# Optimization experiments

Measured on AMD Instinct MI355X. Metric: run time of the kernel, lower is better.

Reference implementation:

```python
import jax, jax.numpy as jnp
import numpy as np

N, E, D, H, C = 50000, 1600000, 256, 8, 32

def setup_inputs() -> dict:
    key = jax.random.key(0)
    ks = jax.random.split(key, 7)
    feat = jax.random.normal(ks[0], (N, D), dtype=jnp.float32)
    edge_weight = jax.random.uniform(ks[1], (E,), dtype=jnp.float32)
    W_lin = jax.random.normal(ks[2], (D, H * C), dtype=jnp.float32) * (1.0 / np.sqrt(D))
    att_l = jax.random.normal(ks[3], (1, H, C), dtype=jnp.float32) * (1.0 / np.sqrt(H))
    att_r = jax.random.normal(ks[4], (1, H, C), dtype=jnp.float32) * (1.0 / np.sqrt(H))
    W_res = jax.random.normal(ks[5], (D, H * C), dtype=jnp.float32) * (1.0 / np.sqrt(D))
    edge_index = jax.random.randint(ks[6], (2, E), 0, N, dtype=jnp.int32)
    return {"feat": feat, "edge_weight": edge_weight, "W_lin": W_lin,
            "att_l": att_l, "att_r": att_r, "W_res": W_res, "edge_index": edge_index}

def reference(feat, edge_weight, W_lin, att_l, att_r, W_res, edge_index):
    n_nodes = feat.shape[0]
    h, c = att_l.shape[1], att_l.shape[2]
    src, dst = edge_index[0], edge_index[1]
    # node projection: [N, H, C]
    x = (feat @ W_lin).reshape(n_nodes, h, c)
    alpha_l = (x * att_l).sum(-1)  # [N, H]
    alpha_r = (x * att_r).sum(-1)  # [N, H]
    # per-edge scores [E, H]
    alpha = alpha_l[src] + alpha_r[dst]
    alpha = edge_weight[:, None] * alpha
    alpha = jnp.where(alpha > 0, alpha, 0.2 * alpha)  # leaky_relu(0.2)
    # segment softmax over destination nodes
    amax = jax.lax.stop_gradient(jax.ops.segment_max(alpha, dst, num_segments=n_nodes))
    ex = jnp.exp(alpha - amax[dst])
    denom = jax.ops.segment_sum(ex, dst, num_segments=n_nodes)
    coeff = ex / (denom[dst] + 1e-16)  # [E, H]
    # weighted message aggregation
    msg = x[src] * coeff[:, :, None]  # [E, H, C]
    agg = jax.ops.segment_sum(msg, dst, num_segments=n_nodes)  # [N, H, C]
    out = jax.nn.elu(agg).reshape(n_nodes, h * c)
    out = out + feat @ W_res  # residual
    return out
```

## Files before the change

kernel.cpp:

```cpp
#include <hip/hip_runtime.h>
#include <stdint.h>

#define D_DIM 256
#define NPAD  640

typedef __bf16 bf16x8 __attribute__((ext_vector_type(8)));
typedef float  f32x4  __attribute__((ext_vector_type(4)));

__device__ __forceinline__ float bf2f(unsigned short u) {
  union { unsigned int i; float f; } cv; cv.i = ((unsigned int)u) << 16; return cv.f;
}
__device__ __forceinline__ unsigned short f2bf(float f) {
  union { float f; unsigned int i; } cv; cv.f = f;
  unsigned int i = cv.i;
  unsigned int lsb = (i >> 16) & 1u;
  i += 0x7fffu + lsb;
  return (unsigned short)(i >> 16);
}
__device__ __forceinline__ void gld16(const void* gptr, void* lptr) {
  __builtin_amdgcn_global_load_lds(
      (const __attribute__((address_space(1))) unsigned int*)gptr,
      (__attribute__((address_space(3))) unsigned int*)lptr, 16, 0, 0);
}

__global__ __launch_bounds__(256) void setup_cvt_prep(
    const float* __restrict__ feat, unsigned short* __restrict__ fb,
    const float* __restrict__ W_lin, const float* __restrict__ W_res,
    const float* __restrict__ att_l, const float* __restrict__ att_r,
    unsigned short* __restrict__ Bt, int nelem, int nb_cvt) {
  int bid = blockIdx.x, t = threadIdx.x;
  if (bid < nb_cvt) {
    int i = (bid * 256 + t) * 8;
    if (i >= nelem) return;
    float4 v0 = *(const float4*)(feat + i);
    float4 v1 = *(const float4*)(feat + i + 4);
    ushort4 a, b;
    a.x = f2bf(v0.x); a.y = f2bf(v0.y); a.z = f2bf(v0.z); a.w = f2bf(v0.w);
    b.x = f2bf(v1.x); b.y = f2bf(v1.y); b.z = f2bf(v1.z); b.w = f2bf(v1.w);
    *(ushort4*)(fb + i) = a;
    *(ushort4*)(fb + i + 4) = b;
  } else {
    int idx = (bid - nb_cvt) * 256 + t;
    int n = idx >> 8, k = idx & 255;
    float v = 0.f;
    if (n < 256) v = W_lin[k * 256 + n];
    else if (n < 512) v = W_res[k * 256 + (n - 256)];
    else if (n < 520) {
      int h = n - 512; float s = 0.f;
      #pragma unroll
      for (int c = 0; c < 32; ++c) s += W_lin[k * 256 + h * 32 + c] * att_l[h * 32 + c];
      v = s;
    } else if (n < 528) {
      int h = n - 520; float s = 0.f;
      #pragma unroll
      for (int c = 0; c < 32; ++c) s += W_lin[k * 256 + h * 32 + c] * att_r[h * 32 + c];
      v = s;
    }
    Bt[idx] = f2bf(v);
  }
}

__global__ __launch_bounds__(256) void scan_partial(const int* __restrict__ cnt,
                                                    int* __restrict__ bsum, int N) {
  __shared__ int s[256];
  int t = threadIdx.x;
  int i = blockIdx.x * 256 + t;
  s[t] = (i < N) ? cnt[i] : 0;
  __syncthreads();
  for (int off = 128; off > 0; off >>= 1) {
    if (t < off) s[t] += s[t + off];
    __syncthreads();
  }
  if (t == 0) bsum[blockIdx.x] = s[0];
}

__global__ __launch_bounds__(256) void scan_top(int* __restrict__ bsum, int nb) {
  __shared__ int s[256];
  int t = threadIdx.x;
  int v = (t < nb) ? bsum[t] : 0;
  s[t] = v;
  __syncthreads();
  for (int off = 1; off < 256; off <<= 1) {
    int u = (t >= off) ? s[t - off] : 0;
    __syncthreads();
    s[t] += u;
    __syncthreads();
  }
  if (t < nb) bsum[t] = s[t] - v;
}

__global__ __launch_bounds__(256) void scan_apply(const int* __restrict__ cnt,
                                                  const int* __restrict__ bsum,
                                                  int* __restrict__ row_ptr, int N) {
  __shared__ int s[256];
  int t = threadIdx.x;
  int i = blockIdx.x * 256 + t;
  int v = (i < N) ? cnt[i] : 0;
  s[t] = v;
  __syncthreads();
  for (int off = 1; off < 256; off <<= 1) {
    int u = (t >= off) ? s[t - off] : 0;
    __syncthreads();
    s[t] += u;
    __syncthreads();
  }
  int excl = bsum[blockIdx.x] + s[t] - v;
  if (i < N) {
    row_ptr[i] = excl;
    if (i == N - 1) row_ptr[N] = excl + v;
  }
}

__global__ __launch_bounds__(256) void gemm_hist(
    const unsigned short* __restrict__ A,
    const unsigned short* __restrict__ Bt,
    float* __restrict__ out, unsigned short* __restrict__ xbf,
    float* __restrict__ alpha_l, float* __restrict__ alpha_r, int M,
    const int* __restrict__ dst, int* __restrict__ cnt, int* __restrict__ rank,
    int E, int nb_hist, int gx) {
  __shared__ unsigned short As[128 * 32];
  __shared__ unsigned short Bs[128 * 32];

  if ((int)blockIdx.x < nb_hist) {
    int base = (int)blockIdx.x * 2048 + threadIdx.x;
    #pragma unroll
    for (int u = 0; u < 8; ++u) {
      int e = base + u * 256;
      if (e < E) rank[e] = atomicAdd(&cnt[dst[e]], 1);
    }
    return;
  }

  int tid  = threadIdx.x;
  int w    = tid >> 6, lane = tid & 63;
  int gb   = (int)blockIdx.x - nb_hist;
  int bm   = (gb % gx) * 128, bn = (gb / gx) * 128;
  int wm   = (w & 1) * 64, wn = (w >> 1) * 64;
  int l16  = lane & 15, quad = lane >> 4;

  f32x4 acc[4][4] = {};

  int srow = w * 32 + (lane >> 2);
  int koff = (lane & 3) * 8;

  for (int k0 = 0; k0 < 256; k0 += 32) {
    #pragma unroll
    for (int i = 0; i < 2; ++i) {
      int r  = srow + i * 16;
      int rg = bm + r; if (rg > M - 1) rg = M - 1;
      gld16(A  + (size_t)rg * 256 + k0 + koff, &As[(w * 32 + i * 16) * 32]);
      gld16(Bt + (size_t)(bn + r) * 256 + k0 + koff, &Bs[(w * 32 + i * 16) * 32]);
    }
    __syncthreads();
    bf16x8 a[4], b[4];
    #pragma unroll
    for (int mi = 0; mi < 4; ++mi)
      a[mi] = *(const bf16x8*)&As[(wm + mi * 16 + l16) * 32 + quad * 8];
    #pragma unroll
    for (int ni = 0; ni < 4; ++ni)
      b[ni] = *(const bf16x8*)&Bs[(wn + ni * 16 + l16) * 32 + quad * 8];
    #pragma unroll
    for (int mi = 0; mi < 4; ++mi)
      #pragma unroll
      for (int ni = 0; ni < 4; ++ni)
        acc[mi][ni] = __builtin_amdgcn_mfma_f32_16x16x32_bf16(a[mi], b[ni], acc[mi][ni], 0, 0, 0);
    __syncthreads();
  }

  #pragma unroll
  for (int mi = 0; mi < 4; ++mi) {
    #pragma unroll
    for (int r = 0; r < 4; ++r) {
      int row = bm + wm + mi * 16 + quad * 4 + r;
      if (row >= M) continue;
      #pragma unroll
      for (int ni = 0; ni < 4; ++ni) {
        int n = bn + wn + ni * 16 + l16;
        float v = acc[mi][ni][r];
        if (n < 256)      xbf[(size_t)row * 256 + n] = f2bf(v);
        else if (n < 512) out[(size_t)row * 256 + (n - 256)] = v;
        else if (n < 520) alpha_l[row * 8 + (n - 512)] = v;
        else if (n < 528) alpha_r[row * 8 + (n - 520)] = v;
      }
    }
  }
}

__global__ __launch_bounds__(256) void scatter_kernel(
    const int* __restrict__ eidx, const float* __restrict__ ew,
    const int* __restrict__ row_ptr, const int* __restrict__ rank,
    const float* __restrict__ alpha_l, const float* __restrict__ alpha_r,
    int* __restrict__ srcA, unsigned short* __restrict__ pexp, int E) {
  int e = blockIdx.x * 256 + threadIdx.x;
  if (e >= E) return;
  int s = eidx[e], d = eidx[E + e];
  int pos = row_ptr[d] + rank[e];
  float w = ew[e];
  float4 al0 = *(const float4*)(alpha_l + (size_t)s * 8);
  float4 al1 = *(const float4*)(alpha_l + (size_t)s * 8 + 4);
  float4 ar0 = *(const float4*)(alpha_r + (size_t)d * 8);
  float4 ar1 = *(const float4*)(alpha_r + (size_t)d * 8 + 4);
  float a[8] = {al0.x + ar0.x, al0.y + ar0.y, al0.z + ar0.z, al0.w + ar0.w,
                al1.x + ar1.x, al1.y + ar1.y, al1.z + ar1.z, al1.w + ar1.w};
  ushort4 o0, o1;
  unsigned short pb[8];
  #pragma unroll
  for (int h = 0; h < 8; ++h) {
    float v = w * a[h];
    v = (v > 0.f) ? v : 0.2f * v;
    pb[h] = f2bf(__expf(v));
  }
  o0.x = pb[0]; o0.y = pb[1]; o0.z = pb[2]; o0.w = pb[3];
  o1.x = pb[4]; o1.y = pb[5]; o1.z = pb[6]; o1.w = pb[7];
  srcA[pos] = s;
  *(ushort4*)(pexp + (size_t)pos * 8) = o0;
  *(ushort4*)(pexp + (size_t)pos * 8 + 4) = o1;
}

__global__ __launch_bounds__(256) void agg_kernel(
    const int* __restrict__ row_ptr, const int* __restrict__ srcA,
    const unsigned short* __restrict__ pexp,
    const unsigned short* __restrict__ xbf, float* __restrict__ out, int N) {
  __shared__ float red[2][64][6];
  int nin  = threadIdx.x >> 7;
  int wv   = (threadIdx.x >> 6) & 1;
  int lane = threadIdx.x & 63;
  int node = blockIdx.x * 2 + nin;
  bool active = node < N;
  int h  = lane >> 3;
  int cb = lane << 2;

  float l = 0.f, ac0 = 0.f, ac1 = 0.f, ac2 = 0.f, ac3 = 0.f;

  if (active) {
    int beg = row_ptr[node], end = row_ptr[node + 1];
    if (beg < end) {
      int last = end - 1;
      const unsigned short* xb = xbf + cb;
      for (int jg = beg + wv * 4; jg < end; jg += 8) {
        int s[4]; float pv[4];
        #pragma unroll
        for (int u = 0; u < 4; ++u) {
          int t = jg + u; t = (t < last) ? t : last;
          s[u]  = srcA[t];
          pv[u] = bf2f(pexp[(size_t)t * 8 + h]);
        }
        ushort4 xv[4];
        #pragma unroll
        for (int u = 0; u < 4; ++u)
          xv[u] = *(const ushort4*)(xb + ((size_t)s[u] << 8));
        #pragma unroll
        for (int u = 0; u < 4; ++u) {
          float p = (jg + u < end) ? pv[u] : 0.f;
          l += p;
          ac0 = fmaf(p, bf2f(xv[u].x), ac0);
          ac1 = fmaf(p, bf2f(xv[u].y), ac1);
          ac2 = fmaf(p, bf2f(xv[u].z), ac2);
          ac3 = fmaf(p, bf2f(xv[u].w), ac3);
        }
      }
    }
  }

  if (wv == 1) {
    red[nin][lane][0] = l;
    red[nin][lane][1] = ac0; red[nin][lane][2] = ac1;
    red[nin][lane][3] = ac2; red[nin][lane][4] = ac3;
  }
  __syncthreads();
  if (active && wv == 0) {
    l   += red[nin][lane][0];
    ac0 += red[nin][lane][1]; ac1 += red[nin][lane][2];
    ac2 += red[nin][lane][3]; ac3 += red[nin][lane][4];
    float r = 1.0f / (l + 1e-16f);
    float o0 = ac0 * r, o1 = ac1 * r, o2 = ac2 * r, o3 = ac3 * r;
    o0 = (o0 > 0.f) ? o0 : expm1f(o0);
    o1 = (o1 > 0.f) ? o1 : expm1f(o1);
    o2 = (o2 > 0.f) ? o2 : expm1f(o2);
    o3 = (o3 > 0.f) ? o3 : expm1f(o3);
    float4* op = (float4*)(out + ((size_t)node << 8) + cb);
    float4 res = *op;
    res.x += o0; res.y += o1; res.z += o2; res.w += o3;
    *op = res;
  }
}

extern "C" void kernel_launch(void* const* d_in, const int* in_sizes, int n_in,
                              void* d_out, int out_size, void* d_ws, size_t ws_size,
                              hipStream_t stream) {
  const float* feat  = (const float*)d_in[0];
  const float* ew    = (const float*)d_in[1];
  const float* W_lin = (const float*)d_in[2];
  const float* att_l = (const float*)d_in[3];
  const float* att_r = (const float*)d_in[4];
  const float* W_res = (const float*)d_in[5];
  const int*   eidx  = (const int*)d_in[6];
  float* out = (float*)d_out;

  int N = in_sizes[0] / D_DIM;
  int E = in_sizes[1];

  char* p = (char*)d_ws;
  auto alloc = [&](size_t bytes) {
    char* r = p; p += (bytes + 255) & ~(size_t)255; return r;
  };
  unsigned short* xbf  = (unsigned short*)alloc((size_t)N * 256 * 2);
  unsigned short* fb   = (unsigned short*)alloc((size_t)N * 256 * 2);
  float* alpha_l       = (float*)alloc((size_t)N * 8 * 4);
  float* alpha_r       = (float*)alloc((size_t)N * 8 * 4);
  unsigned short* Bt   = (unsigned short*)alloc((size_t)NPAD * D_DIM * 2);
  int*   row_ptr       = (int*)alloc((size_t)(N + 1) * 4);
  int*   cnt           = (int*)alloc((size_t)N * 4);
  int*   rank          = (int*)alloc((size_t)E * 4);
  int*   bsum          = (int*)alloc(1024);
  int*   srcA          = (int*)alloc((size_t)E * 4);
  unsigned short* pexp_sep = (unsigned short*)alloc((size_t)E * 8 * 2);
  bool sep_ok = ((size_t)((char*)(pexp_sep + (size_t)E * 8) - (char*)d_ws) <= ws_size);
  unsigned short* pexp = sep_ok ? pexp_sep : fb;

  int nb      = (N + 255) / 256;
  int nb_cvt  = (N * 256 / 8 + 255) / 256;
  int nb_prep = NPAD * D_DIM / 256;
  int nb_hist = (E + 2047) / 2048;
  int nb_scat = (E + 255) / 256;
  int gx = (N + 127) / 128;
  int gemm_blocks = gx * (NPAD / 128);

  hipMemsetAsync(cnt, 0, (size_t)N * 4, stream);

  setup_cvt_prep<<<nb_cvt + nb_prep, 256, 0, stream>>>(
      feat, fb, W_lin, W_res, att_l, att_r, Bt, N * 256, nb_cvt);

  gemm_hist<<<nb_hist + gemm_blocks, 256, 0, stream>>>(
      fb, Bt, out, xbf, alpha_l, alpha_r, N,
      eidx + E, cnt, rank, E, nb_hist, gx);

  scan_partial<<<nb, 256, 0, stream>>>(cnt, bsum, N);
  scan_top<<<1, 256, 0, stream>>>(bsum, nb);
  scan_apply<<<nb, 256, 0, stream>>>(cnt, bsum, row_ptr, N);

  scatter_kernel<<<nb_scat, 256, 0, stream>>>(
      eidx, ew, row_ptr, rank, alpha_l, alpha_r, srcA, pexp, E);

  agg_kernel<<<(N + 1) / 2, 256, 0, stream>>>(row_ptr, srcA, pexp, xbf, out, N);
}
```

Baseline: 457.8 us.

## Move histogram into setup kernel and widen GEMM K-tile with swizzled LDS

The edge-histogram atomics move out of the GEMM launch and into the fused setup/convert kernel, so the GEMM kernel no longer carries the histogram branch and its blocks. The GEMM K-tile grows from 32 to 64, halving the number of barrier-separated iterations. An XOR swizzle on the LDS column offsets is meant to avoid bank conflicts on the fragment reads. In exchange the GEMM uses twice the LDS per block, which may reduce occupancy, and the histogram now competes with the conversion pass inside the setup launch.

```diff
diff --git a/kernel.cpp b/kernel.cpp
--- a/kernel.cpp
+++ b/kernel.cpp
@@ -23,12 +23,23 @@
       (__attribute__((address_space(3))) unsigned int*)lptr, 16, 0, 0);
 }
 
-__global__ __launch_bounds__(256) void setup_cvt_prep(
+__global__ __launch_bounds__(256) void setup_fused(
     const float* __restrict__ feat, unsigned short* __restrict__ fb,
     const float* __restrict__ W_lin, const float* __restrict__ W_res,
     const float* __restrict__ att_l, const float* __restrict__ att_r,
-    unsigned short* __restrict__ Bt, int nelem, int nb_cvt) {
+    unsigned short* __restrict__ Bt, int nelem, int nb_hist, int nb_cvt,
+    const int* __restrict__ dst, int* __restrict__ cnt, int* __restrict__ rank, int E) {
   int bid = blockIdx.x, t = threadIdx.x;
+  if (bid < nb_hist) {
+    int base = bid * 2048 + t;
+    #pragma unroll
+    for (int u = 0; u < 8; ++u) {
+      int e = base + u * 256;
+      if (e < E) rank[e] = atomicAdd(&cnt[dst[e]], 1);
+    }
+    return;
+  }
+  bid -= nb_hist;
   if (bid < nb_cvt) {
     int i = (bid * 256 + t) * 8;
     if (i >= nelem) return;
@@ -111,59 +122,56 @@
   }
 }
 
-__global__ __launch_bounds__(256) void gemm_hist(
+__global__ __launch_bounds__(256) void gemm_kernel(
     const unsigned short* __restrict__ A,
     const unsigned short* __restrict__ Bt,
     float* __restrict__ out, unsigned short* __restrict__ xbf,
-    float* __restrict__ alpha_l, float* __restrict__ alpha_r, int M,
-    const int* __restrict__ dst, int* __restrict__ cnt, int* __restrict__ rank,
-    int E, int nb_hist, int gx) {
-  __shared__ unsigned short As[128 * 32];
-  __shared__ unsigned short Bs[128 * 32];
-
-  if ((int)blockIdx.x < nb_hist) {
-    int base = (int)blockIdx.x * 2048 + threadIdx.x;
-    #pragma unroll
-    for (int u = 0; u < 8; ++u) {
-      int e = base + u * 256;
-      if (e < E) rank[e] = atomicAdd(&cnt[dst[e]], 1);
-    }
-    return;
-  }
+    float* __restrict__ alpha_l, float* __restrict__ alpha_r, int M, int gx) {
+  __shared__ unsigned short As[128 * 64];
+  __shared__ unsigned short Bs[128 * 64];
 
   int tid  = threadIdx.x;
   int w    = tid >> 6, lane = tid & 63;
-  int gb   = (int)blockIdx.x - nb_hist;
+  int gb   = (int)blockIdx.x;
   int bm   = (gb % gx) * 128, bn = (gb / gx) * 128;
   int wm   = (w & 1) * 64, wn = (w >> 1) * 64;
   int l16  = lane & 15, quad = lane >> 4;
 
   f32x4 acc[4][4] = {};
 
-  int srow = w * 32 + (lane >> 2);
-  int koff = (lane & 3) * 8;
-
-  for (int k0 = 0; k0 < 256; k0 += 32) {
+  int sr8     = lane >> 3;
+  int koff_sw = (((lane & 7) ^ sr8) * 8);
+
+  for (int k0 = 0; k0 < 256; k0 += 64) {
     #pragma unroll
-    for (int i = 0; i < 2; ++i) {
-      int r  = srow + i * 16;
-      int rg = bm + r; if (rg > M - 1) rg = M - 1;
-      gld16(A  + (size_t)rg * 256 + k0 + koff, &As[(w * 32 + i * 16) * 32]);
-      gld16(Bt + (size_t)(bn + r) * 256 + k0 + koff, &Bs[(w * 32 + i * 16) * 32]);
-    }
-    __syncthreads();
-    bf16x8 a[4], b[4];
+    for (int j = 0; j < 4; ++j) {
+      int rbase = w * 32 + j * 8;
+      int rga = bm + rbase + sr8; if (rga > M - 1) rga = M - 1;
+      gld16(A  + (size_t)rga * 256 + k0 + koff_sw, &As[rbase * 64]);
+      gld16(Bt + (size_t)(bn + rbase + sr8) * 256 + k0 + koff_sw, &Bs[rbase * 64]);
+    }
+    __syncthreads();
     #pragma unroll
-    for (int mi = 0; mi < 4; ++mi)
-      a[mi] = *(const bf16x8*)&As[(wm + mi * 16 + l16) * 32 + quad * 8];
-    #pragma unroll
-    for (int ni = 0; ni < 4; ++ni)
-      b[ni] = *(const bf16x8*)&Bs[(wn + ni * 16 + l16) * 32 + quad * 8];
-    #pragma unroll
-    for (int mi = 0; mi < 4; ++mi)
-      #pragma unroll
-      for (int ni = 0; ni < 4; ++ni)
-        acc[mi][ni] = __builtin_amdgcn_mfma_f32_16x16x32_bf16(a[mi], b[ni], acc[mi][ni], 0, 0, 0);
+    for (int kk = 0; kk < 64; kk += 32) {
+      bf16x8 a[4], b[4];
+      #pragma unroll
+      for (int mi = 0; mi < 4; ++mi) {
+        int r = wm + mi * 16 + l16;
+        int col = (kk * 2 + quad * 16) ^ ((r & 7) << 4);
+        a[mi] = *(const bf16x8*)((const char*)&As[r * 64] + col);
+      }
+      #pragma unroll
+      for (int ni = 0; ni < 4; ++ni) {
+        int r = wn + ni * 16 + l16;
+        int col = (kk * 2 + quad * 16) ^ ((r & 7) << 4);
+        b[ni] = *(const bf16x8*)((const char*)&Bs[r * 64] + col);
+      }
+      #pragma unroll
+      for (int mi = 0; mi < 4; ++mi)
+        #pragma unroll
+        for (int ni = 0; ni < 4; ++ni)
+          acc[mi][ni] = __builtin_amdgcn_mfma_f32_16x16x32_bf16(a[mi], b[ni], acc[mi][ni], 0, 0, 0);
+    }
     __syncthreads();
   }
 
@@ -202,7 +210,6 @@
   float4 ar1 = *(const float4*)(alpha_r + (size_t)d * 8 + 4);
   float a[8] = {al0.x + ar0.x, al0.y + ar0.y, al0.z + ar0.z, al0.w + ar0.w,
                 al1.x + ar1.x, al1.y + ar1.y, al1.z + ar1.z, al1.w + ar1.w};
-  ushort4 o0, o1;
   unsigned short pb[8];
   #pragma unroll
   for (int h = 0; h < 8; ++h) {
@@ -210,6 +217,7 @@
     v = (v > 0.f) ? v : 0.2f * v;
     pb[h] = f2bf(__expf(v));
   }
+  ushort4 o0, o1;
   o0.x = pb[0]; o0.y = pb[1]; o0.z = pb[2]; o0.w = pb[3];
   o1.x = pb[4]; o1.y = pb[5]; o1.z = pb[6]; o1.w = pb[7];
   srcA[pos] = s;
@@ -314,9 +322,9 @@
   int*   rank          = (int*)alloc((size_t)E * 4);
   int*   bsum          = (int*)alloc(1024);
   int*   srcA          = (int*)alloc((size_t)E * 4);
-  unsigned short* pexp_sep = (unsigned short*)alloc((size_t)E * 8 * 2);
-  bool sep_ok = ((size_t)((char*)(pexp_sep + (size_t)E * 8) - (char*)d_ws) <= ws_size);
-  unsigned short* pexp = sep_ok ? pexp_sep : fb;
+  unsigned short* pexp = (unsigned short*)alloc((size_t)E * 8 * 2);
+
+  if ((size_t)(p - (char*)d_ws) > ws_size) pexp = fb;
 
   int nb      = (N + 255) / 256;
   int nb_cvt  = (N * 256 / 8 + 255) / 256;
@@ -328,12 +336,12 @@
 
   hipMemsetAsync(cnt, 0, (size_t)N * 4, stream);
 
-  setup_cvt_prep<<<nb_cvt + nb_prep, 256, 0, stream>>>(
-      feat, fb, W_lin, W_res, att_l, att_r, Bt, N * 256, nb_cvt);
-
-  gemm_hist<<<nb_hist + gemm_blocks, 256, 0, stream>>>(
-      fb, Bt, out, xbf, alpha_l, alpha_r, N,
-      eidx + E, cnt, rank, E, nb_hist, gx);
+  setup_fused<<<nb_hist + nb_cvt + nb_prep, 256, 0, stream>>>(
+      feat, fb, W_lin, W_res, att_l, att_r, Bt, N * 256, nb_hist, nb_cvt,
+      eidx + E, cnt, rank, E);
+
+  gemm_kernel<<<gemm_blocks, 256, 0, stream>>>(
+      fb, Bt, out, xbf, alpha_l, alpha_r, N, gx);
 
   scan_partial<<<nb, 256, 0, stream>>>(cnt, bsum, N);
   scan_top<<<1, 256, 0, stream>>>(bsum, nb);
```

After: 445.9 us. -2.6%, faster.
